# Performance work log

Hardware: AMD Instinct MI355X
Metric: run time of the kernel (lower is better)

## Reference

```python
import jax, jax.numpy as jnp
import numpy as np

N_NODES = 10000
N_EDGES = 640000
HIDDEN = 128
N_LAYERS = 3
DECAY_RATE = 1.0


def setup_inputs() -> dict:
    key = jax.random.key(0)
    ks = jax.random.split(key, 16)
    D, L = HIDDEN, N_LAYERS
    s = 1.0 / np.sqrt(D)
    inp = {
        "x": jax.random.normal(ks[0], (N_NODES, D), dtype=jnp.float32),
        "edge_index": jax.random.randint(ks[1], (2, N_EDGES), 0, N_NODES, dtype=jnp.int32),
        "confidences": jax.random.uniform(ks[2], (N_NODES,), dtype=jnp.float32),
        # per-layer message MLP params, stacked over layers: [L, D, D] / [L, D]
        "msg_W1": jax.random.normal(ks[3], (L, D, D), dtype=jnp.float32) * s,
        "msg_b1": jnp.zeros((L, D), dtype=jnp.float32),
        "msg_W2": jax.random.normal(ks[4], (L, D, D), dtype=jnp.float32) * s,
        "msg_b2": jnp.zeros((L, D), dtype=jnp.float32),
        # per-layer self MLP params
        "self_W1": jax.random.normal(ks[5], (L, D, D), dtype=jnp.float32) * s,
        "self_b1": jnp.zeros((L, D), dtype=jnp.float32),
        "self_W2": jax.random.normal(ks[6], (L, D, D), dtype=jnp.float32) * s,
        "self_b2": jnp.zeros((L, D), dtype=jnp.float32),
        # layer-importance score net: Linear(D,D) -> ReLU -> Linear(D,1)
        "score_W1": jax.random.normal(ks[7], (D, D), dtype=jnp.float32) * s,
        "score_b1": jnp.zeros((D,), dtype=jnp.float32),
        "score_W2": jax.random.normal(ks[8], (D, 1), dtype=jnp.float32) * s,
        "score_b2": jnp.zeros((1,), dtype=jnp.float32),
    }
    return inp


def _mlp2(h, W1, b1, W2, b2):
    return jax.nn.relu(h @ W1 + b1) @ W2 + b2


def reference(x, edge_index, confidences,
              msg_W1, msg_b1, msg_W2, msg_b2,
              self_W1, self_b1, self_W2, self_b2,
              score_W1, score_b1, score_W2, score_b2):
    src, dst = edge_index[0], edge_index[1]
    # confidence-weighted edge weights: exp(-decay * |c_src - c_dst|)
    edge_weights = jnp.exp(-DECAY_RATE * jnp.abs(confidences[src] - confidences[dst]))  # [E]

    h = x
    layer_outputs = []
    for i in range(N_LAYERS):
        messages = _mlp2(h[src], msg_W1[i], msg_b1[i], msg_W2[i], msg_b2[i])  # [E, D]
        messages = messages * edge_weights[:, None]
        aggr = jax.ops.segment_sum(messages, dst, num_segments=N_NODES)  # [N, D]
        self_loop = _mlp2(h, self_W1[i], self_b1[i], self_W2[i], self_b2[i])
        h = jax.nn.relu(aggr + self_loop)  # dropout is identity in eval mode
        layer_outputs.append(h)

    stacked = jnp.stack(layer_outputs, axis=0)  # [L, N, D]
    scores = _mlp2(stacked, score_W1, score_b1, score_W2, score_b2)[..., 0]  # [L, N]
    layer_weights = jax.nn.softmax(scores, axis=0)  # softmax over layers
    output = jnp.sum(layer_weights[:, :, None] * stacked, axis=0)  # [N, D]
    return output, stacked, layer_weights
```

## Files before the change

### kernel.cpp

```cpp
#include <hip/hip_runtime.h>

#define NN 10000
#define NE 640000
#define D 128
#define NF (NN * D)
#define WS 136
#define WBYTES (D * WS * 2)
#define WCHUNKS (WBYTES / 1024)
#define NBLK 100
#define EPB (NE / NBLK)
#define MPAD 1000000
#define GB32 313

typedef __bf16 bf16x8 __attribute__((ext_vector_type(8)));
typedef __bf16 bf16x2 __attribute__((ext_vector_type(2)));
typedef float f32x4 __attribute__((ext_vector_type(4)));

__device__ __forceinline__ void async_copy16(const void* g, void* l) {
    __builtin_amdgcn_global_load_lds(
        (const __attribute__((address_space(1))) unsigned int*)g,
        (__attribute__((address_space(3))) unsigned int*)l, 16, 0, 0);
}


__global__ __launch_bounds__(256) void hist_prep_kernel(
    const int* __restrict__ ei, int* __restrict__ cnt_blk, int* __restrict__ local_rank,
    const float2* __restrict__ x2, bf16x2* __restrict__ xbf,
    const float* __restrict__ mW1, const float* __restrict__ mW2,
    const float* __restrict__ sW1, const float* __restrict__ sW2,
    const float* __restrict__ scW1, __bf16* __restrict__ wt) {
    __shared__ unsigned int hist[NN / 2];
    int b = blockIdx.x, t = threadIdx.x;
    if (b < NBLK) {
        for (int i = t; i < NN / 2; i += 256) hist[i] = 0u;
        __syncthreads();
        int base = b * EPB;
#pragma unroll 1
        for (int i = 0; i < EPB / 256; i++) {
            int e = base + i * 256 + t;
            int d = ei[NE + e];
            int sh = (d & 1) * 16;
            unsigned int old = atomicAdd(&hist[d >> 1], 1u << sh);
            local_rank[e] = (old >> sh) & 0xFFFFu;
        }
        __syncthreads();
        for (int i = t; i < NN; i += 256)
            cnt_blk[b * NN + i] = (hist[i >> 1] >> ((i & 1) * 16)) & 0xFFFFu;
    } else if (b < NBLK + 2500) {
        int i = (b - NBLK) * 256 + t;
        float2 v = x2[i];
        bf16x2 o;
        o.x = (__bf16)v.x;
        o.y = (__bf16)v.y;
        xbf[i] = o;
    } else {
        int m = b - (NBLK + 2500);
        const float* W = (m < 3)   ? mW1 + (size_t)m * D * D
                       : (m < 6)   ? mW2 + (size_t)(m - 3) * D * D
                       : (m < 9)   ? sW1 + (size_t)(m - 6) * D * D
                       : (m < 12)  ? sW2 + (size_t)(m - 9) * D * D
                                   : scW1;
        __bf16* o = wt + (size_t)m * D * WS;
        for (int i = t; i < D * D; i += 256) {
            int k = i >> 7, n = i & 127;
            o[n * WS + k] = (__bf16)W[i];
        }
    }
}

__global__ void scan_kernel(const int* __restrict__ cnt, int* __restrict__ row_ptr) {
    __shared__ int lds[256];
    int t = threadIdx.x;
    const int CH = (NN + 255) / 256;
    int base = t * CH;
    int s = 0;
    for (int i = 0; i < CH; i++) {
        int idx = base + i;
        if (idx < NN) s += (cnt[idx] + 31) & ~31;
    }
    lds[t] = s;
    __syncthreads();
    for (int off = 1; off < 256; off <<= 1) {
        int v = (t >= off) ? lds[t - off] : 0;
        __syncthreads();
        lds[t] += v;
        __syncthreads();
    }
    int run = (t == 0) ? 0 : lds[t - 1];
    for (int i = 0; i < CH; i++) {
        int idx = base + i;
        if (idx < NN) {
            row_ptr[idx] = run;
            run += (cnt[idx] + 31) & ~31;
        }
    }
    if (t == 255) row_ptr[NN] = lds[255];
}

__global__ void scatter_kernel(const int* __restrict__ ei, const float* __restrict__ conf,
                               const int* __restrict__ local_rank,
                               const int* __restrict__ cnt_blk,
                               const int* __restrict__ row_ptr, float2* __restrict__ meta) {
    int e = blockIdx.x * 256 + threadIdx.x;
    if (e >= NE) return;
    int s = ei[e];
    int d = ei[NE + e];
    int blk = e / EPB;
    int pos = row_ptr[d] + cnt_blk[blk * NN + d] + local_rank[e];
    meta[pos] = make_float2(__int_as_float(s), expf(-fabsf(conf[s] - conf[d])));
}


__global__ __launch_bounds__(128) void mlp_pair_mfma(
    const __bf16* __restrict__ Abf,
    const __bf16* __restrict__ Wt1a, const float* __restrict__ b1a,
    const __bf16* __restrict__ Wt2a, const float* __restrict__ b2a, __bf16* __restrict__ Mbf,
    const __bf16* __restrict__ Wt1b, const float* __restrict__ b1b,
    const __bf16* __restrict__ Wt2b, const float* __restrict__ b2b, float* __restrict__ Cself) {
    const __bf16* Wt1 = blockIdx.y ? Wt1b : Wt1a;
    const float* b1 = blockIdx.y ? b1b : b1a;
    const __bf16* Wt2 = blockIdx.y ? Wt2b : Wt2a;
    const float* b2 = blockIdx.y ? b2b : b2a;

    __shared__ __align__(16) __bf16 Wl[2][D * WS];
    __shared__ __align__(16) __bf16 Tl[2][16 * WS];
    int t = threadIdx.x;
    int wid = t >> 6, lane = t & 63;
    int m16 = lane & 15, q = lane >> 4;

    for (int c = wid; c < WCHUNKS; c += 2)
        async_copy16((const char*)Wt1 + c * 1024 + lane * 16,
                     (char*)&Wl[0][0] + c * 1024 + lane * 16);

    int row0 = blockIdx.x * 32 + wid * 16;
    int arow = min(row0 + m16, NN - 1);

    bf16x8 af[4];
#pragma unroll
    for (int kk = 0; kk < 4; kk++) af[kk] = *(const bf16x8*)&Abf[(size_t)arow * D + kk * 32 + q * 8];
    float b1v[8], b2v[8];
#pragma unroll
    for (int ct = 0; ct < 8; ct++) { b1v[ct] = b1[ct * 16 + m16]; b2v[ct] = b2[ct * 16 + m16]; }

    __syncthreads();

    for (int c = wid; c < WCHUNKS; c += 2)
        async_copy16((const char*)Wt2 + c * 1024 + lane * 16,
                     (char*)&Wl[1][0] + c * 1024 + lane * 16);

    f32x4 acc[8];
#pragma unroll
    for (int ct = 0; ct < 8; ct++) acc[ct] = (f32x4){0.f, 0.f, 0.f, 0.f};
#pragma unroll
    for (int kk = 0; kk < 4; kk++) {
#pragma unroll
        for (int ct = 0; ct < 8; ct++) {
            bf16x8 b = *(const bf16x8*)&Wl[0][(ct * 16 + m16) * WS + kk * 32 + q * 8];
            acc[ct] = __builtin_amdgcn_mfma_f32_16x16x32_bf16(af[kk], b, acc[ct], 0, 0, 0);
        }
    }
#pragma unroll
    for (int ct = 0; ct < 8; ct++) {
#pragma unroll
        for (int r = 0; r < 4; r++) {
            float v = fmaxf(acc[ct][r] + b1v[ct], 0.f);
            Tl[wid][(q * 4 + r) * WS + ct * 16 + m16] = (__bf16)v;
        }
    }
    __syncthreads();

#pragma unroll
    for (int ct = 0; ct < 8; ct++) acc[ct] = (f32x4){0.f, 0.f, 0.f, 0.f};
#pragma unroll
    for (int kk = 0; kk < 4; kk++) {
        bf16x8 a = *(const bf16x8*)&Tl[wid][m16 * WS + kk * 32 + q * 8];
#pragma unroll
        for (int ct = 0; ct < 8; ct++) {
            bf16x8 b = *(const bf16x8*)&Wl[1][(ct * 16 + m16) * WS + kk * 32 + q * 8];
            acc[ct] = __builtin_amdgcn_mfma_f32_16x16x32_bf16(a, b, acc[ct], 0, 0, 0);
        }
    }
    if (blockIdx.y == 0) {
#pragma unroll
        for (int ct = 0; ct < 8; ct++) {
#pragma unroll
            for (int r = 0; r < 4; r++) {
                int row = row0 + q * 4 + r;
                if (row < NN) Mbf[(size_t)row * D + ct * 16 + m16] = (__bf16)(acc[ct][r] + b2v[ct]);
            }
        }
    } else {
#pragma unroll
        for (int ct = 0; ct < 8; ct++) {
#pragma unroll
            for (int r = 0; r < 4; r++) {
                int row = row0 + q * 4 + r;
                if (row < NN) Cself[(size_t)row * D + ct * 16 + m16] = acc[ct][r] + b2v[ct];
            }
        }
    }
}


__global__ __launch_bounds__(128) void mlp0_colsum_kernel(
    const __bf16* __restrict__ Abf,
    const __bf16* __restrict__ Wt1a, const float* __restrict__ b1a,
    const __bf16* __restrict__ Wt2a, const float* __restrict__ b2a, __bf16* __restrict__ Mbf,
    const __bf16* __restrict__ Wt1b, const float* __restrict__ b1b,
    const __bf16* __restrict__ Wt2b, const float* __restrict__ b2b, float* __restrict__ Cself,
    int* __restrict__ cnt_blk, int* __restrict__ cnt) {
    __shared__ __align__(16) __bf16 Wl[2][D * WS];
    __shared__ __align__(16) __bf16 Tl[2][16 * WS];
    int b = blockIdx.x, t = threadIdx.x;

    if (b >= 2 * GB32) {
        int n = (b - 2 * GB32) * 128 + t;
        if (n >= NN) return;
        int acc = 0;
#pragma unroll 4
        for (int blk = 0; blk < NBLK; blk++) {
            int v = cnt_blk[blk * NN + n];
            cnt_blk[blk * NN + n] = acc;
            acc += v;
        }
        cnt[n] = acc;
        return;
    }

    int pb = (b >= GB32);
    int bx = pb ? b - GB32 : b;
    const __bf16* Wt1 = pb ? Wt1b : Wt1a;
    const float* b1 = pb ? b1b : b1a;
    const __bf16* Wt2 = pb ? Wt2b : Wt2a;
    const float* b2 = pb ? b2b : b2a;

    int wid = t >> 6, lane = t & 63;
    int m16 = lane & 15, q = lane >> 4;

    for (int c = wid; c < WCHUNKS; c += 2)
        async_copy16((const char*)Wt1 + c * 1024 + lane * 16,
                     (char*)&Wl[0][0] + c * 1024 + lane * 16);

    int row0 = bx * 32 + wid * 16;
    int arow = min(row0 + m16, NN - 1);

    bf16x8 af[4];
#pragma unroll
    for (int kk = 0; kk < 4; kk++) af[kk] = *(const bf16x8*)&Abf[(size_t)arow * D + kk * 32 + q * 8];
    float b1v[8], b2v[8];
#pragma unroll
    for (int ct = 0; ct < 8; ct++) { b1v[ct] = b1[ct * 16 + m16]; b2v[ct] = b2[ct * 16 + m16]; }

    __syncthreads();

    for (int c = wid; c < WCHUNKS; c += 2)
        async_copy16((const char*)Wt2 + c * 1024 + lane * 16,
                     (char*)&Wl[1][0] + c * 1024 + lane * 16);

    f32x4 acc[8];
#pragma unroll
    for (int ct = 0; ct < 8; ct++) acc[ct] = (f32x4){0.f, 0.f, 0.f, 0.f};
#pragma unroll
    for (int kk = 0; kk < 4; kk++) {
#pragma unroll
        for (int ct = 0; ct < 8; ct++) {
            bf16x8 bb = *(const bf16x8*)&Wl[0][(ct * 16 + m16) * WS + kk * 32 + q * 8];
            acc[ct] = __builtin_amdgcn_mfma_f32_16x16x32_bf16(af[kk], bb, acc[ct], 0, 0, 0);
        }
    }
#pragma unroll
    for (int ct = 0; ct < 8; ct++) {
#pragma unroll
        for (int r = 0; r < 4; r++) {
            float v = fmaxf(acc[ct][r] + b1v[ct], 0.f);
            Tl[wid][(q * 4 + r) * WS + ct * 16 + m16] = (__bf16)v;
        }
    }
    __syncthreads();

#pragma unroll
    for (int ct = 0; ct < 8; ct++) acc[ct] = (f32x4){0.f, 0.f, 0.f, 0.f};
#pragma unroll
    for (int kk = 0; kk < 4; kk++) {
        bf16x8 a = *(const bf16x8*)&Tl[wid][m16 * WS + kk * 32 + q * 8];
#pragma unroll
        for (int ct = 0; ct < 8; ct++) {
            bf16x8 bb = *(const bf16x8*)&Wl[1][(ct * 16 + m16) * WS + kk * 32 + q * 8];
            acc[ct] = __builtin_amdgcn_mfma_f32_16x16x32_bf16(a, bb, acc[ct], 0, 0, 0);
        }
    }
    if (pb == 0) {
#pragma unroll
        for (int ct = 0; ct < 8; ct++) {
#pragma unroll
            for (int r = 0; r < 4; r++) {
                int row = row0 + q * 4 + r;
                if (row < NN) Mbf[(size_t)row * D + ct * 16 + m16] = (__bf16)(acc[ct][r] + b2v[ct]);
            }
        }
    } else {
#pragma unroll
        for (int ct = 0; ct < 8; ct++) {
#pragma unroll
            for (int r = 0; r < 4; r++) {
                int row = row0 + q * 4 + r;
                if (row < NN) Cself[(size_t)row * D + ct * 16 + m16] = acc[ct][r] + b2v[ct];
            }
        }
    }
}


__global__ __launch_bounds__(256) void aggregate_kernel(
    const uint4* __restrict__ Mbf4, const float4* __restrict__ Mself4,
    const int* __restrict__ row_ptr, const float2* __restrict__ meta,
    float4* __restrict__ out4, bf16x8* __restrict__ stbf8) {
    int wid = (blockIdx.x * 256 + threadIdx.x) >> 6;
    int lane = threadIdx.x & 63;
    int q = lane >> 4, l4 = lane & 15, l5 = lane & 31;
    int beg = row_ptr[wid], end = row_ptr[wid + 1];
    float a[8] = {0.f, 0.f, 0.f, 0.f, 0.f, 0.f, 0.f, 0.f};
    float2 mcur = meta[beg + l5];
    for (int j = beg; j < end; j += 32) {
        float2 mnext = meta[j + 32 + l5];
        int srcid[8];
        float wgt[8];
#pragma unroll
        for (int u = 0; u < 8; u++) {
            int sl = 4 * u + q;
            srcid[u] = __float_as_int(__shfl(mcur.x, sl));
            wgt[u] = __shfl(mcur.y, sl);
        }
        uint4 g[8];
#pragma unroll
        for (int u = 0; u < 8; u++) g[u] = Mbf4[(size_t)srcid[u] * 16 + l4];
#pragma unroll
        for (int u = 0; u < 8; u++) {
            float w = wgt[u];
            a[0] = fmaf(w, __uint_as_float(g[u].x << 16), a[0]);
            a[1] = fmaf(w, __uint_as_float(g[u].x & 0xFFFF0000u), a[1]);
            a[2] = fmaf(w, __uint_as_float(g[u].y << 16), a[2]);
            a[3] = fmaf(w, __uint_as_float(g[u].y & 0xFFFF0000u), a[3]);
            a[4] = fmaf(w, __uint_as_float(g[u].z << 16), a[4]);
            a[5] = fmaf(w, __uint_as_float(g[u].z & 0xFFFF0000u), a[5]);
            a[6] = fmaf(w, __uint_as_float(g[u].w << 16), a[6]);
            a[7] = fmaf(w, __uint_as_float(g[u].w & 0xFFFF0000u), a[7]);
        }
        mcur = mnext;
    }
#pragma unroll
    for (int i = 0; i < 8; i++) {
        a[i] += __shfl_xor(a[i], 16);
        a[i] += __shfl_xor(a[i], 32);
    }
    if (q == 0) {
        float4 sv0 = Mself4[(size_t)wid * 32 + 2 * l4];
        float4 sv1 = Mself4[(size_t)wid * 32 + 2 * l4 + 1];
        float4 r0, r1;
        r0.x = fmaxf(a[0] + sv0.x, 0.f);
        r0.y = fmaxf(a[1] + sv0.y, 0.f);
        r0.z = fmaxf(a[2] + sv0.z, 0.f);
        r0.w = fmaxf(a[3] + sv0.w, 0.f);
        r1.x = fmaxf(a[4] + sv1.x, 0.f);
        r1.y = fmaxf(a[5] + sv1.y, 0.f);
        r1.z = fmaxf(a[6] + sv1.z, 0.f);
        r1.w = fmaxf(a[7] + sv1.w, 0.f);
        out4[(size_t)wid * 32 + 2 * l4] = r0;
        out4[(size_t)wid * 32 + 2 * l4 + 1] = r1;
        bf16x8 hb;
        hb[0] = (__bf16)r0.x; hb[1] = (__bf16)r0.y;
        hb[2] = (__bf16)r0.z; hb[3] = (__bf16)r0.w;
        hb[4] = (__bf16)r1.x; hb[5] = (__bf16)r1.y;
        hb[6] = (__bf16)r1.z; hb[7] = (__bf16)r1.w;
        stbf8[(size_t)wid * 16 + l4] = hb;
    }
}


__global__ __launch_bounds__(256) void score_finalize_mfma(
    const __bf16* __restrict__ stbf, const float* __restrict__ st,
    const __bf16* __restrict__ Wt1, const float* __restrict__ b1,
    const float* __restrict__ w2, const float* __restrict__ b2,
    float* __restrict__ out, float* __restrict__ lw_out) {
    __shared__ __align__(16) __bf16 Wl[D * WS];
    __shared__ float sc_l[3][64];
    __shared__ float lw_l[3][64];
    int t = threadIdx.x;
    int wid = t >> 6, lane = t & 63;
    int m16 = lane & 15, q = lane >> 4;
    int row0 = blockIdx.x * 64;

    for (int c = wid; c < WCHUNKS; c += 4)
        async_copy16((const char*)Wt1 + c * 1024 + lane * 16,
                     (char*)&Wl[0] + c * 1024 + lane * 16);
    __syncthreads();

    int arow = min(row0 + wid * 16 + m16, NN - 1);
    float bb = b2[0];

    for (int l = 0; l < 3; l++) {
        const __bf16* A = stbf + (size_t)l * NF;
        f32x4 acc[8];
#pragma unroll
        for (int ct = 0; ct < 8; ct++) acc[ct] = (f32x4){0.f, 0.f, 0.f, 0.f};
#pragma unroll
        for (int kk = 0; kk < 4; kk++) {
            bf16x8 a = *(const bf16x8*)&A[(size_t)arow * D + kk * 32 + q * 8];
#pragma unroll
            for (int ct = 0; ct < 8; ct++) {
                bf16x8 b = *(const bf16x8*)&Wl[(ct * 16 + m16) * WS + kk * 32 + q * 8];
                acc[ct] = __builtin_amdgcn_mfma_f32_16x16x32_bf16(a, b, acc[ct], 0, 0, 0);
            }
        }
        float p[4] = {0.f, 0.f, 0.f, 0.f};
#pragma unroll
        for (int ct = 0; ct < 8; ct++) {
            float bv = b1[ct * 16 + m16];
            float wv = w2[ct * 16 + m16];
#pragma unroll
            for (int r = 0; r < 4; r++) p[r] += fmaxf(acc[ct][r] + bv, 0.f) * wv;
        }
#pragma unroll
        for (int r = 0; r < 4; r++) {
#pragma unroll
            for (int off = 1; off < 16; off <<= 1) p[r] += __shfl_xor(p[r], off);
            if (m16 == 0) sc_l[l][wid * 16 + q * 4 + r] = p[r] + bb;
        }
    }
    __syncthreads();

    if (t < 64) {
        int row = row0 + t;
        float s0 = sc_l[0][t], s1 = sc_l[1][t], s2 = sc_l[2][t];
        float m = fmaxf(s0, fmaxf(s1, s2));
        float e0 = expf(s0 - m), e1 = expf(s1 - m), e2 = expf(s2 - m);
        float inv = 1.f / (e0 + e1 + e2);
        lw_l[0][t] = e0 * inv;
        lw_l[1][t] = e1 * inv;
        lw_l[2][t] = e2 * inv;
        if (row < NN) {
            lw_out[row] = e0 * inv;
            lw_out[NN + row] = e1 * inv;
            lw_out[2 * NN + row] = e2 * inv;
        }
    }
    __syncthreads();

    for (int i = t; i < 64 * 32; i += 256) {
        int r = i >> 5, c4 = i & 31;
        int row = row0 + r;
        if (row >= NN) break;
        float4 v0 = ((const float4*)(st + (size_t)row * D))[c4];
        float4 v1 = ((const float4*)(st + (size_t)NF + (size_t)row * D))[c4];
        float4 v2 = ((const float4*)(st + 2 * (size_t)NF + (size_t)row * D))[c4];
        float w0 = lw_l[0][r], w1 = lw_l[1][r], w2v = lw_l[2][r];
        float4 o;
        o.x = w0 * v0.x + w1 * v1.x + w2v * v2.x;
        o.y = w0 * v0.y + w1 * v1.y + w2v * v2.y;
        o.z = w0 * v0.z + w1 * v1.z + w2v * v2.z;
        o.w = w0 * v0.w + w1 * v1.w + w2v * v2.w;
        ((float4*)(out + (size_t)row * D))[c4] = o;
    }
}

extern "C" void kernel_launch(void* const* d_in, const int* in_sizes, int n_in,
                              void* d_out, int out_size, void* d_ws, size_t ws_size,
                              hipStream_t stream) {
    const float* x = (const float*)d_in[0];
    const int* ei = (const int*)d_in[1];
    const float* conf = (const float*)d_in[2];
    const float* msg_W1 = (const float*)d_in[3];
    const float* msg_b1 = (const float*)d_in[4];
    const float* msg_W2 = (const float*)d_in[5];
    const float* msg_b2 = (const float*)d_in[6];
    const float* self_W1 = (const float*)d_in[7];
    const float* self_b1 = (const float*)d_in[8];
    const float* self_W2 = (const float*)d_in[9];
    const float* self_b2 = (const float*)d_in[10];
    const float* score_W1 = (const float*)d_in[11];
    const float* score_b1 = (const float*)d_in[12];
    const float* score_W2 = (const float*)d_in[13];
    const float* score_b2 = (const float*)d_in[14];

    float* out = (float*)d_out;
    float* out_stacked = out + NF;
    float* out_lw = out + 4 * (size_t)NF;

    float* w = (float*)d_ws;
    float* Mself = w;
    float2* meta = (float2*)(w + (size_t)NF);
    __bf16* xbf = (__bf16*)(meta + MPAD);
    __bf16* stbf = xbf + (size_t)NF;
    __bf16* Mbf = stbf + 3 * (size_t)NF;
    __bf16* wt = Mbf + (size_t)NF;
    int* local_rank = (int*)(wt + 13 * (size_t)D * WS);
    int* cnt_blk = local_rank + NE;
    int* row_ptr = cnt_blk + NBLK * NN;
    int* cnt = row_ptr + NN + 1;

    const size_t MAT = (size_t)D * WS;
    const int GE = (NE + 255) / 256;
    const int GB64 = (NN + 63) / 64;
    const int GCS = (NN + 127) / 128;

    hipMemsetAsync(meta, 0, (size_t)MPAD * sizeof(float2), stream);
    hist_prep_kernel<<<NBLK + 2513, 256, 0, stream>>>(ei, cnt_blk, local_rank,
                                                      (const float2*)x, (bf16x2*)xbf,
                                                      msg_W1, msg_W2, self_W1, self_W2,
                                                      score_W1, wt);
    mlp0_colsum_kernel<<<2 * GB32 + GCS, 128, 0, stream>>>(
        xbf,
        wt + 0 * MAT, msg_b1, wt + 3 * MAT, msg_b2, Mbf,
        wt + 6 * MAT, self_b1, wt + 9 * MAT, self_b2, Mself,
        cnt_blk, cnt);
    scan_kernel<<<1, 256, 0, stream>>>(cnt, row_ptr);
    scatter_kernel<<<GE, 256, 0, stream>>>(ei, conf, local_rank, cnt_blk, row_ptr, meta);
    aggregate_kernel<<<NN / 4, 256, 0, stream>>>(
        (const uint4*)Mbf, (const float4*)Mself, row_ptr, meta,
        (float4*)(out_stacked + 0 * (size_t)NF), (bf16x8*)(stbf + 0 * (size_t)NF));

    for (int l = 1; l < 3; l++) {
        const __bf16* a_in = stbf + (size_t)(l - 1) * NF;
        mlp_pair_mfma<<<dim3(GB32, 2), 128, 0, stream>>>(
            a_in,
            wt + (size_t)l * MAT, msg_b1 + (size_t)l * D,
            wt + (size_t)(3 + l) * MAT, msg_b2 + (size_t)l * D, Mbf,
            wt + (size_t)(6 + l) * MAT, self_b1 + (size_t)l * D,
            wt + (size_t)(9 + l) * MAT, self_b2 + (size_t)l * D, Mself);
        aggregate_kernel<<<NN / 4, 256, 0, stream>>>(
            (const uint4*)Mbf, (const float4*)Mself, row_ptr, meta,
            (float4*)(out_stacked + (size_t)l * NF),
            (bf16x8*)(stbf + (size_t)l * NF));
    }

    score_finalize_mfma<<<GB64, 256, 0, stream>>>(
        stbf, out_stacked, wt + 12 * MAT, score_b1, score_W2, score_b2, out, out_lw);
}
```

Measured before the change: 251.8 us.

## Fold meta memset into prep kernel and scan into colsum via last-block counter

Replaces the separate hipMemsetAsync of the edge metadata buffer with extra zeroing blocks inside the histogram/prep kernel. It also removes the standalone single-block scan kernel: the last column-sum block, found through an atomic done counter, runs the row_ptr prefix scan. This cuts two launches and their gaps, but the scan runs on a single 128-thread block at the tail of the MLP kernel, and a bounds check is added to scatter.

```diff
diff --git a/kernel.cpp b/kernel.cpp
--- a/kernel.cpp
+++ b/kernel.cpp
@@ -11,6 +11,8 @@
 #define EPB (NE / NBLK)
 #define MPAD 1000000
 #define GB32 313
+#define NCS ((NN + 127) / 128)
+#define MZB ((MPAD / 2 + 1023) / 1024)
 
 typedef __bf16 bf16x8 __attribute__((ext_vector_type(8)));
 typedef __bf16 bf16x2 __attribute__((ext_vector_type(2)));
@@ -28,9 +30,11 @@
     const float2* __restrict__ x2, bf16x2* __restrict__ xbf,
     const float* __restrict__ mW1, const float* __restrict__ mW2,
     const float* __restrict__ sW1, const float* __restrict__ sW2,
-    const float* __restrict__ scW1, __bf16* __restrict__ wt) {
+    const float* __restrict__ scW1, __bf16* __restrict__ wt,
+    float4* __restrict__ metaz, int* __restrict__ done_ctr) {
     __shared__ unsigned int hist[NN / 2];
     int b = blockIdx.x, t = threadIdx.x;
+    if (b == 0 && t == 0) *done_ctr = 0;
     if (b < NBLK) {
         for (int i = t; i < NN / 2; i += 256) hist[i] = 0u;
         __syncthreads();
@@ -53,7 +57,7 @@
         o.x = (__bf16)v.x;
         o.y = (__bf16)v.y;
         xbf[i] = o;
-    } else {
+    } else if (b < NBLK + 2513) {
         int m = b - (NBLK + 2500);
         const float* W = (m < 3)   ? mW1 + (size_t)m * D * D
                        : (m < 6)   ? mW2 + (size_t)(m - 3) * D * D
@@ -65,36 +69,14 @@
             int k = i >> 7, n = i & 127;
             o[n * WS + k] = (__bf16)W[i];
         }
-    }
-}
-
-__global__ void scan_kernel(const int* __restrict__ cnt, int* __restrict__ row_ptr) {
-    __shared__ int lds[256];
-    int t = threadIdx.x;
-    const int CH = (NN + 255) / 256;
-    int base = t * CH;
-    int s = 0;
-    for (int i = 0; i < CH; i++) {
-        int idx = base + i;
-        if (idx < NN) s += (cnt[idx] + 31) & ~31;
-    }
-    lds[t] = s;
-    __syncthreads();
-    for (int off = 1; off < 256; off <<= 1) {
-        int v = (t >= off) ? lds[t - off] : 0;
-        __syncthreads();
-        lds[t] += v;
-        __syncthreads();
-    }
-    int run = (t == 0) ? 0 : lds[t - 1];
-    for (int i = 0; i < CH; i++) {
-        int idx = base + i;
-        if (idx < NN) {
-            row_ptr[idx] = run;
-            run += (cnt[idx] + 31) & ~31;
-        }
-    }
-    if (t == 255) row_ptr[NN] = lds[255];
+    } else {
+        int base = (b - (NBLK + 2513)) * 1024 + t;
+#pragma unroll
+        for (int i = 0; i < 4; i++) {
+            int idx = base + i * 256;
+            if (idx < MPAD / 2) metaz[idx] = make_float4(0.f, 0.f, 0.f, 0.f);
+        }
+    }
 }
 
 __global__ void scatter_kernel(const int* __restrict__ ei, const float* __restrict__ conf,
@@ -107,7 +89,8 @@
     int d = ei[NE + e];
     int blk = e / EPB;
     int pos = row_ptr[d] + cnt_blk[blk * NN + d] + local_rank[e];
-    meta[pos] = make_float2(__int_as_float(s), expf(-fabsf(conf[s] - conf[d])));
+    if (pos >= 0 && pos < MPAD)
+        meta[pos] = make_float2(__int_as_float(s), expf(-fabsf(conf[s] - conf[d])));
 }
 
 
@@ -208,22 +191,56 @@
     const __bf16* __restrict__ Wt2a, const float* __restrict__ b2a, __bf16* __restrict__ Mbf,
     const __bf16* __restrict__ Wt1b, const float* __restrict__ b1b,
     const __bf16* __restrict__ Wt2b, const float* __restrict__ b2b, float* __restrict__ Cself,
-    int* __restrict__ cnt_blk, int* __restrict__ cnt) {
+    int* __restrict__ cnt_blk, int* __restrict__ cnt,
+    int* __restrict__ row_ptr, int* __restrict__ done_ctr) {
     __shared__ __align__(16) __bf16 Wl[2][D * WS];
     __shared__ __align__(16) __bf16 Tl[2][16 * WS];
+    __shared__ int scan_aux[129];
     int b = blockIdx.x, t = threadIdx.x;
 
     if (b >= 2 * GB32) {
         int n = (b - 2 * GB32) * 128 + t;
-        if (n >= NN) return;
-        int acc = 0;
+        if (n < NN) {
+            int acc = 0;
 #pragma unroll 4
-        for (int blk = 0; blk < NBLK; blk++) {
-            int v = cnt_blk[blk * NN + n];
-            cnt_blk[blk * NN + n] = acc;
-            acc += v;
-        }
-        cnt[n] = acc;
+            for (int blk = 0; blk < NBLK; blk++) {
+                int v = cnt_blk[blk * NN + n];
+                cnt_blk[blk * NN + n] = acc;
+                acc += v;
+            }
+            cnt[n] = acc;
+        }
+        __threadfence();
+        __syncthreads();
+        if (t == 0) scan_aux[128] = atomicAdd(done_ctr, 1);
+        __syncthreads();
+        if (scan_aux[128] == NCS - 1) {
+            __threadfence();
+            const int CH2 = (NN + 127) / 128;
+            int base = t * CH2;
+            int s = 0;
+            for (int i = 0; i < CH2; i++) {
+                int idx = base + i;
+                if (idx < NN) s += (cnt[idx] + 31) & ~31;
+            }
+            scan_aux[t] = s;
+            __syncthreads();
+            for (int off = 1; off < 128; off <<= 1) {
+                int v = (t >= off) ? scan_aux[t - off] : 0;
+                __syncthreads();
+                scan_aux[t] += v;
+                __syncthreads();
+            }
+            int run = (t == 0) ? 0 : scan_aux[t - 1];
+            for (int i = 0; i < CH2; i++) {
+                int idx = base + i;
+                if (idx < NN) {
+                    row_ptr[idx] = run;
+                    run += (cnt[idx] + 31) & ~31;
+                }
+            }
+            if (t == 127) row_ptr[NN] = scan_aux[127];
+        }
         return;
     }
 
@@ -497,23 +514,21 @@
     int* cnt_blk = local_rank + NE;
     int* row_ptr = cnt_blk + NBLK * NN;
     int* cnt = row_ptr + NN + 1;
+    int* done_ctr = cnt + NN;
 
     const size_t MAT = (size_t)D * WS;
     const int GE = (NE + 255) / 256;
     const int GB64 = (NN + 63) / 64;
-    const int GCS = (NN + 127) / 128;
-
-    hipMemsetAsync(meta, 0, (size_t)MPAD * sizeof(float2), stream);
-    hist_prep_kernel<<<NBLK + 2513, 256, 0, stream>>>(ei, cnt_blk, local_rank,
-                                                      (const float2*)x, (bf16x2*)xbf,
-                                                      msg_W1, msg_W2, self_W1, self_W2,
-                                                      score_W1, wt);
-    mlp0_colsum_kernel<<<2 * GB32 + GCS, 128, 0, stream>>>(
+
+    hist_prep_kernel<<<NBLK + 2513 + MZB, 256, 0, stream>>>(
+        ei, cnt_blk, local_rank, (const float2*)x, (bf16x2*)xbf,
+        msg_W1, msg_W2, self_W1, self_W2, score_W1, wt,
+        (float4*)meta, done_ctr);
+    mlp0_colsum_kernel<<<2 * GB32 + NCS, 128, 0, stream>>>(
         xbf,
         wt + 0 * MAT, msg_b1, wt + 3 * MAT, msg_b2, Mbf,
         wt + 6 * MAT, self_b1, wt + 9 * MAT, self_b2, Mself,
-        cnt_blk, cnt);
-    scan_kernel<<<1, 256, 0, stream>>>(cnt, row_ptr);
+        cnt_blk, cnt, row_ptr, done_ctr);
     scatter_kernel<<<GE, 256, 0, stream>>>(ei, conf, local_rank, cnt_blk, row_ptr, meta);
     aggregate_kernel<<<NN / 4, 256, 0, stream>>>(
         (const uint4*)Mbf, (const float4*)Mself, row_ptr, meta,
```

After: 263.2 us. 1.05x slower.

## Fuse meta memset into prep kernel, preload both MLP weights, reorder colsum blocks

Applied to the files above, without the earlier changes.

Replaces the separate hipMemsetAsync of the meta buffer with extra zeroing blocks in hist_prep_kernel, which saves one launch. Both MLP weight matrices are now loaded asynchronously into LDS before the first barrier, and the second barrier is removed so the second GEMM no longer waits on a separate weight load. The column-sum blocks are moved to the front of the grid and their loads are batched in groups of 25 for more memory-level parallelism. Dropping the __syncthreads after the Tl writes relies on each wave reading only its own Tl slice.

```diff
diff --git a/kernel.cpp b/kernel.cpp
--- a/kernel.cpp
+++ b/kernel.cpp
@@ -11,6 +11,8 @@
 #define EPB (NE / NBLK)
 #define MPAD 1000000
 #define GB32 313
+#define NCS ((NN + 127) / 128)
+#define MZB ((MPAD / 2 + 1023) / 1024)
 
 typedef __bf16 bf16x8 __attribute__((ext_vector_type(8)));
 typedef __bf16 bf16x2 __attribute__((ext_vector_type(2)));
@@ -28,7 +30,8 @@
     const float2* __restrict__ x2, bf16x2* __restrict__ xbf,
     const float* __restrict__ mW1, const float* __restrict__ mW2,
     const float* __restrict__ sW1, const float* __restrict__ sW2,
-    const float* __restrict__ scW1, __bf16* __restrict__ wt) {
+    const float* __restrict__ scW1, __bf16* __restrict__ wt,
+    float4* __restrict__ metaz) {
     __shared__ unsigned int hist[NN / 2];
     int b = blockIdx.x, t = threadIdx.x;
     if (b < NBLK) {
@@ -53,7 +56,7 @@
         o.x = (__bf16)v.x;
         o.y = (__bf16)v.y;
         xbf[i] = o;
-    } else {
+    } else if (b < NBLK + 2513) {
         int m = b - (NBLK + 2500);
         const float* W = (m < 3)   ? mW1 + (size_t)m * D * D
                        : (m < 6)   ? mW2 + (size_t)(m - 3) * D * D
@@ -64,6 +67,13 @@
         for (int i = t; i < D * D; i += 256) {
             int k = i >> 7, n = i & 127;
             o[n * WS + k] = (__bf16)W[i];
+        }
+    } else {
+        int base = (b - (NBLK + 2513)) * 1024 + t;
+#pragma unroll
+        for (int i = 0; i < 4; i++) {
+            int idx = base + i * 256;
+            if (idx < MPAD / 2) metaz[idx] = make_float4(0.f, 0.f, 0.f, 0.f);
         }
     }
 }
@@ -128,9 +138,11 @@
     int wid = t >> 6, lane = t & 63;
     int m16 = lane & 15, q = lane >> 4;
 
-    for (int c = wid; c < WCHUNKS; c += 2)
-        async_copy16((const char*)Wt1 + c * 1024 + lane * 16,
-                     (char*)&Wl[0][0] + c * 1024 + lane * 16);
+    for (int c = wid; c < 2 * WCHUNKS; c += 2) {
+        const char* src = (c < WCHUNKS) ? (const char*)Wt1 + c * 1024
+                                        : (const char*)Wt2 + (c - WCHUNKS) * 1024;
+        async_copy16(src + lane * 16, (char*)&Wl[0][0] + c * 1024 + lane * 16);
+    }
 
     int row0 = blockIdx.x * 32 + wid * 16;
     int arow = min(row0 + m16, NN - 1);
@@ -143,10 +155,6 @@
     for (int ct = 0; ct < 8; ct++) { b1v[ct] = b1[ct * 16 + m16]; b2v[ct] = b2[ct * 16 + m16]; }
 
     __syncthreads();
-
-    for (int c = wid; c < WCHUNKS; c += 2)
-        async_copy16((const char*)Wt2 + c * 1024 + lane * 16,
-                     (char*)&Wl[1][0] + c * 1024 + lane * 16);
 
     f32x4 acc[8];
 #pragma unroll
@@ -167,7 +175,6 @@
             Tl[wid][(q * 4 + r) * WS + ct * 16 + m16] = (__bf16)v;
         }
     }
-    __syncthreads();
 
 #pragma unroll
     for (int ct = 0; ct < 8; ct++) acc[ct] = (f32x4){0.f, 0.f, 0.f, 0.f};
@@ -213,22 +220,28 @@
     __shared__ __align__(16) __bf16 Tl[2][16 * WS];
     int b = blockIdx.x, t = threadIdx.x;
 
-    if (b >= 2 * GB32) {
-        int n = (b - 2 * GB32) * 128 + t;
+    if (b < NCS) {
+        int n = b * 128 + t;
         if (n >= NN) return;
         int acc = 0;
-#pragma unroll 4
-        for (int blk = 0; blk < NBLK; blk++) {
-            int v = cnt_blk[blk * NN + n];
-            cnt_blk[blk * NN + n] = acc;
-            acc += v;
+#pragma unroll
+        for (int g = 0; g < 4; g++) {
+            int v[25];
+#pragma unroll
+            for (int k = 0; k < 25; k++) v[k] = cnt_blk[(g * 25 + k) * NN + n];
+#pragma unroll
+            for (int k = 0; k < 25; k++) {
+                cnt_blk[(g * 25 + k) * NN + n] = acc;
+                acc += v[k];
+            }
         }
         cnt[n] = acc;
         return;
     }
 
-    int pb = (b >= GB32);
-    int bx = pb ? b - GB32 : b;
+    int mb = b - NCS;
+    int pb = (mb >= GB32);
+    int bx = pb ? mb - GB32 : mb;
     const __bf16* Wt1 = pb ? Wt1b : Wt1a;
     const float* b1 = pb ? b1b : b1a;
     const __bf16* Wt2 = pb ? Wt2b : Wt2a;
@@ -237,9 +250,11 @@
     int wid = t >> 6, lane = t & 63;
     int m16 = lane & 15, q = lane >> 4;
 
-    for (int c = wid; c < WCHUNKS; c += 2)
-        async_copy16((const char*)Wt1 + c * 1024 + lane * 16,
-                     (char*)&Wl[0][0] + c * 1024 + lane * 16);
+    for (int c = wid; c < 2 * WCHUNKS; c += 2) {
+        const char* src = (c < WCHUNKS) ? (const char*)Wt1 + c * 1024
+                                        : (const char*)Wt2 + (c - WCHUNKS) * 1024;
+        async_copy16(src + lane * 16, (char*)&Wl[0][0] + c * 1024 + lane * 16);
+    }
 
     int row0 = bx * 32 + wid * 16;
     int arow = min(row0 + m16, NN - 1);
@@ -252,10 +267,6 @@
     for (int ct = 0; ct < 8; ct++) { b1v[ct] = b1[ct * 16 + m16]; b2v[ct] = b2[ct * 16 + m16]; }
 
     __syncthreads();
-
-    for (int c = wid; c < WCHUNKS; c += 2)
-        async_copy16((const char*)Wt2 + c * 1024 + lane * 16,
-                     (char*)&Wl[1][0] + c * 1024 + lane * 16);
 
     f32x4 acc[8];
 #pragma unroll
@@ -276,7 +287,6 @@
             Tl[wid][(q * 4 + r) * WS + ct * 16 + m16] = (__bf16)v;
         }
     }
-    __syncthreads();
 
 #pragma unroll
     for (int ct = 0; ct < 8; ct++) acc[ct] = (f32x4){0.f, 0.f, 0.f, 0.f};
@@ -501,14 +511,12 @@
     const size_t MAT = (size_t)D * WS;
     const int GE = (NE + 255) / 256;
     const int GB64 = (NN + 63) / 64;
-    const int GCS = (NN + 127) / 128;
-
-    hipMemsetAsync(meta, 0, (size_t)MPAD * sizeof(float2), stream);
-    hist_prep_kernel<<<NBLK + 2513, 256, 0, stream>>>(ei, cnt_blk, local_rank,
-                                                      (const float2*)x, (bf16x2*)xbf,
-                                                      msg_W1, msg_W2, self_W1, self_W2,
-                                                      score_W1, wt);
-    mlp0_colsum_kernel<<<2 * GB32 + GCS, 128, 0, stream>>>(
+
+    hist_prep_kernel<<<NBLK + 2513 + MZB, 256, 0, stream>>>(
+        ei, cnt_blk, local_rank, (const float2*)x, (bf16x2*)xbf,
+        msg_W1, msg_W2, self_W1, self_W2, score_W1, wt,
+        (float4*)meta);
+    mlp0_colsum_kernel<<<NCS + 2 * GB32, 128, 0, stream>>>(
         xbf,
         wt + 0 * MAT, msg_b1, wt + 3 * MAT, msg_b2, Mbf,
         wt + 6 * MAT, self_b1, wt + 9 * MAT, self_b2, Mself,
```

After: 244.6 us. -2.9%, faster.
